# Kernel optimization log

Hardware: AMD Instinct MI355X
Metric: run time of the kernel (lower is better)

## Reference

```python
import jax, jax.numpy as jnp
import numpy as np
import math

IN_DIM = 1024
L = 4096
D_MODEL = 512
D_INNER = 1024   # expand=2 * d_model
D_STATE = 16
D_CONV = 4
DT_RANK = 32     # ceil(d_model / 16)
N_LAYERS = 2
RATE = 10


def setup_inputs() -> dict:
    key = jax.random.key(0)
    ks = iter(jax.random.split(key, 32))
    def w(shape, fan_in):
        return jax.random.normal(next(ks), shape, jnp.float32) * (1.0 / math.sqrt(fan_in))
    return {
        "x": jax.random.normal(next(ks), (1, L, IN_DIM), jnp.float32),
        "rate": RATE,
        "fc1_w": w((D_MODEL, IN_DIM), IN_DIM),
        "fc1_b": jnp.zeros((D_MODEL,), jnp.float32),
        "ln_w": jnp.ones((N_LAYERS, D_MODEL), jnp.float32),
        "ln_b": jnp.zeros((N_LAYERS, D_MODEL), jnp.float32),
        "in_proj_w": w((N_LAYERS, 2 * D_INNER, D_MODEL), D_MODEL),
        "conv_w": w((N_LAYERS, D_INNER, D_CONV), D_CONV),
        "conv_b": jnp.zeros((N_LAYERS, D_INNER), jnp.float32),
        "x_proj_w": w((N_LAYERS, DT_RANK + 2 * D_STATE, D_INNER), D_INNER),
        "dt_proj_w": w((N_LAYERS, D_INNER, DT_RANK), DT_RANK),
        "dt_proj_b": jax.random.normal(next(ks), (N_LAYERS, D_INNER), jnp.float32) * 0.1,
        "A_log": jnp.tile(jnp.log(jnp.arange(1, D_STATE + 1, dtype=jnp.float32)), (N_LAYERS, D_INNER, 1)),
        "D_skip": jnp.ones((N_LAYERS, D_INNER), jnp.float32),
        "out_proj_w": w((N_LAYERS, D_MODEL, D_INNER), D_INNER),
        "norm_w": jnp.ones((D_MODEL,), jnp.float32),
        "norm_b": jnp.zeros((D_MODEL,), jnp.float32),
        "attn_w1": w((128, D_MODEL), D_MODEL),
        "attn_b1": jnp.zeros((128,), jnp.float32),
        "attn_w2": w((1, 128), 128),
        "attn_b2": jnp.zeros((1,), jnp.float32),
        "out2048_w": w((2048, D_MODEL), D_MODEL),
        "out2048_b": jnp.zeros((2048,), jnp.float32),
    }


def _layernorm(x, w, b, eps=1e-5):
    mu = x.mean(-1, keepdims=True)
    var = ((x - mu) ** 2).mean(-1, keepdims=True)
    return (x - mu) * jax.lax.rsqrt(var + eps) * w + b


def _causal_conv(x, w, b):
    # depthwise causal conv: x [L, d], w [d, K] -> y[t, d] = sum_k w[d, k] * x[t - (K-1) + k, d]
    K = w.shape[1]
    xp = jnp.pad(x, ((K - 1, 0), (0, 0)))
    y = sum(xp[k:k + x.shape[0]] * w[:, k] for k in range(K))
    return y + b


def _selective_scan(u, dt, A, B, C, Dp, z):
    # u, dt, z: [L, d]; A: [d, n]; B, C: [L, n]; Dp: [d]
    def step(h, inp):
        dt_t, B_t, C_t, u_t = inp
        dA = jnp.exp(dt_t[:, None] * A)                    # [d, n]
        h = dA * h + (dt_t * u_t)[:, None] * B_t[None, :]  # [d, n]
        return h, h @ C_t                                  # y_t: [d]
    h0 = jnp.zeros((u.shape[1], A.shape[1]), u.dtype)
    _, y = jax.lax.scan(step, h0, (dt, B, C, u))
    return (y + u * Dp) * jax.nn.silu(z)


def _srmamba(h, perm, inv, in_w, cw, cb, xw, dtw, dtb, A_log, Dp, ow):
    xz = h @ in_w.T                         # [L, 2*d_inner]
    x, z = jnp.split(xz, 2, axis=-1)
    x, z = x[perm], z[perm]                 # sequence reordering (stride `rate`)
    x = jax.nn.silu(_causal_conv(x, cw, cb))
    dbl = x @ xw.T                          # [L, dt_rank + 2n]
    dt = jax.nn.softplus(dbl[:, :DT_RANK] @ dtw.T + dtb)
    B = dbl[:, DT_RANK:DT_RANK + D_STATE]
    C = dbl[:, DT_RANK + D_STATE:]
    y = _selective_scan(x, dt, -jnp.exp(A_log), B, C, Dp, z)
    return y[inv] @ ow.T                    # restore original order, out_proj


def reference(x, rate, fc1_w, fc1_b, ln_w, ln_b, in_proj_w, conv_w, conv_b, x_proj_w, dt_proj_w, dt_proj_b, A_log, D_skip, out_proj_w, norm_w, norm_b, attn_w1, attn_b1, attn_w2, attn_b2, out2048_w, out2048_b):
    h = jax.nn.relu(x[0] @ fc1_w.T + fc1_b)   # [L, 512]
    Lx = h.shape[0]
    perm = jnp.concatenate([jnp.arange(i, Lx, rate) for i in range(rate)])
    inv = jnp.argsort(perm)
    for l in range(N_LAYERS):
        h = h + _srmamba(_layernorm(h, ln_w[l], ln_b[l]), perm, inv,
                         in_proj_w[l], conv_w[l], conv_b[l], x_proj_w[l],
                         dt_proj_w[l], dt_proj_b[l], A_log[l], D_skip[l], out_proj_w[l])
    h = _layernorm(h, norm_w, norm_b)
    a = jnp.tanh(h @ attn_w1.T + attn_b1) @ attn_w2.T + attn_b2  # [L, 1]
    Aatt = jax.nn.softmax(a[:, 0])                                # [L]
    pooled = Aatt @ h                                             # [512]
    out = pooled @ out2048_w.T + out2048_b                        # [2048]
    return out[None, :], Aatt[None, None, :]
```

## Files before the change

kernel.cpp:

```cpp
#include <hip/hip_runtime.h>
#include <hip/hip_fp16.h>
#include <math.h>

#define L 4096
#define DIN 1024
#define DM 512
#define DI 1024
#define DS 16
#define DTR 32
#define NCH 128
#define CHK 32

typedef _Float16 v8h __attribute__((ext_vector_type(8)));
typedef float v4f __attribute__((ext_vector_type(4)));

__global__ void perm_k(int* __restrict__ perm, const int* __restrict__ ratep) {
    int p = blockIdx.x * blockDim.x + threadIdx.x;
    if (p >= L) return;
    int rate = ratep[0];
    int cum = 0;
    for (int g = 0; g < rate; ++g) {
        int sz = (L - g + rate - 1) / rate;
        if (p < cum + sz) { perm[p] = g + rate * (p - cum); return; }
        cum += sz;
    }
}

__global__ __launch_bounds__(256) void f2h_k(
    const float* __restrict__ in, _Float16* __restrict__ out)
{
    int i = (blockIdx.x * 256 + threadIdx.x) * 4;
    float4 v = *(const float4*)(in + i);
    _Float16 h4[4] = {(_Float16)v.x, (_Float16)v.y, (_Float16)v.z, (_Float16)v.w};
    *(uint2*)(out + i) = *(uint2*)h4;
}

__global__ __launch_bounds__(256) void zero4_k(float* __restrict__ p) {
    int i = (blockIdx.x * 256 + threadIdx.x) * 4;
    *(float4*)(p + i) = make_float4(0.f, 0.f, 0.f, 0.f);
}

template<int ACT, int BNT>
__global__ __launch_bounds__(256) void hgemm_nt(
    const _Float16* __restrict__ A, int lda,
    const _Float16* __restrict__ B, int ldb,
    float* __restrict__ C, int ldc,
    const float* __restrict__ bias, int K, int accum)
{
    constexpr int MI = (BNT == 128) ? 4 : 2;
    __shared__ _Float16 As[128][40];
    __shared__ _Float16 Bs[BNT][40];
    int tid = threadIdx.x;
    int m0 = blockIdx.y * 128, n0 = blockIdx.x * BNT;
    int lane = tid & 63, wave = tid >> 6;
    int wm, wn;
    if constexpr (BNT == 128) { wm = (wave >> 1) * 64; wn = (wave & 1) * 64; }
    else                      { wm = wave * 32;        wn = 0; }
    int quad = lane >> 4, r16 = lane & 15;
    v4f acc[MI][4] = {};

    int srow = tid >> 1;
    int scol = (tid & 1) * 16;
    const _Float16* Ag = A + (size_t)(m0 + srow) * lda + scol;
    int srowB = (BNT == 128) ? srow : (tid >> 2);
    int scolB = (BNT == 128) ? scol : (tid & 3) * 8;
    const _Float16* Bg = B + (size_t)(n0 + srowB) * ldb + scolB;

    uint4 a0, a1, b0, b1;
    a0 = *(const uint4*)(Ag);
    a1 = *(const uint4*)(Ag + 8);
    b0 = *(const uint4*)(Bg);
    if constexpr (BNT == 128) b1 = *(const uint4*)(Bg + 8);

    int KS = K / 32;
    for (int ks = 0; ks < KS; ++ks) {
        __syncthreads();
        *(uint4*)&As[srow][scol] = a0;
        *(uint4*)&As[srow][scol + 8] = a1;
        *(uint4*)&Bs[srowB][scolB] = b0;
        if constexpr (BNT == 128) *(uint4*)&Bs[srowB][scolB + 8] = b1;
        __syncthreads();
        if (ks + 1 < KS) {
            int k0 = (ks + 1) * 32;
            a0 = *(const uint4*)(Ag + k0);
            a1 = *(const uint4*)(Ag + k0 + 8);
            b0 = *(const uint4*)(Bg + k0);
            if constexpr (BNT == 128) b1 = *(const uint4*)(Bg + k0 + 8);
        }
        v8h af[MI], bf[4];
#pragma unroll
        for (int i = 0; i < MI; ++i)
            af[i] = *(const v8h*)&As[wm + i * 16 + r16][quad * 8];
#pragma unroll
        for (int j = 0; j < 4; ++j)
            bf[j] = *(const v8h*)&Bs[wn + j * 16 + r16][quad * 8];
#pragma unroll
        for (int i = 0; i < MI; ++i)
#pragma unroll
            for (int j = 0; j < 4; ++j)
                acc[i][j] = __builtin_amdgcn_mfma_f32_16x16x32_f16(
                    af[i], bf[j], acc[i][j], 0, 0, 0);
    }

#pragma unroll
    for (int i = 0; i < MI; ++i) {
#pragma unroll
        for (int j = 0; j < 4; ++j) {
            int col = n0 + wn + j * 16 + r16;
            int rbase = m0 + wm + i * 16 + quad * 4;
            float bv = bias ? bias[col] : 0.f;
#pragma unroll
            for (int r = 0; r < 4; ++r) {
                float v = acc[i][j][r] + bv;
                if (ACT == 1) v = fmaxf(v, 0.f);
                float* p = C + (size_t)(rbase + r) * ldc + col;
                if (accum) v += *p;
                *p = v;
            }
        }
    }
}

#define BM 64
#define BN 64
#define BKK 32
template<int ACT>
__global__ __launch_bounds__(256) void gemm_nt(
    const float* __restrict__ A, int lda,
    const float* __restrict__ B, int ldb,
    float* __restrict__ C, int ldc,
    const float* __restrict__ bias,
    int M, int N, int K, int kchunk, int accum)
{
    __shared__ float As[BKK][BM + 4];
    __shared__ float Bs[BKK][BN + 4];
    int tid = threadIdx.x;
    int m0 = blockIdx.y * BM;
    int n0 = blockIdx.x * BN;
    int tx = tid & 15, ty = tid >> 4;
    float acc[4][4] = {};
    int arow = tid >> 3;
    int ak = (tid & 7) * 4;
    int kb = blockIdx.z * kchunk;
    int ke = min(K, kb + kchunk);

    for (int k0 = kb; k0 < ke; k0 += BKK) {
#pragma unroll
        for (int r = 0; r < 2; ++r) {
            int row = arow + r * 32;
            float4 va = *(const float4*)(A + (size_t)(m0 + row) * lda + k0 + ak);
            As[ak + 0][row] = va.x; As[ak + 1][row] = va.y;
            As[ak + 2][row] = va.z; As[ak + 3][row] = va.w;
            float4 vb = *(const float4*)(B + (size_t)(n0 + row) * ldb + k0 + ak);
            Bs[ak + 0][row] = vb.x; Bs[ak + 1][row] = vb.y;
            Bs[ak + 2][row] = vb.z; Bs[ak + 3][row] = vb.w;
        }
        __syncthreads();
#pragma unroll
        for (int kk = 0; kk < BKK; ++kk) {
            float4 a4 = *(const float4*)&As[kk][ty * 4];
            float4 b4 = *(const float4*)&Bs[kk][tx * 4];
            float a[4] = {a4.x, a4.y, a4.z, a4.w};
            float b[4] = {b4.x, b4.y, b4.z, b4.w};
#pragma unroll
            for (int i = 0; i < 4; ++i)
#pragma unroll
                for (int j = 0; j < 4; ++j)
                    acc[i][j] = fmaf(a[i], b[j], acc[i][j]);
        }
        __syncthreads();
    }

#pragma unroll
    for (int i = 0; i < 4; ++i) {
        int row = m0 + ty * 4 + i;
        int col = n0 + tx * 4;
        float* cp = C + (size_t)row * ldc + col;
        if (accum == 2) {
#pragma unroll
            for (int j = 0; j < 4; ++j) atomicAdd(cp + j, acc[i][j]);
            continue;
        }
        float v[4];
#pragma unroll
        for (int j = 0; j < 4; ++j) {
            float x = acc[i][j] + (bias ? bias[col + j] : 0.f);
            if (ACT == 2) x = (x > 20.f) ? x : log1pf(expf(x));
            else if (ACT == 3) x = tanhf(x);
            v[j] = x;
        }
        if (accum == 1) {
#pragma unroll
            for (int j = 0; j < 4; ++j) v[j] += cp[j];
        }
#pragma unroll
        for (int j = 0; j < 4; ++j) cp[j] = v[j];
    }
}

__global__ __launch_bounds__(256) void layernorm_k(
    const float* __restrict__ x, const float* __restrict__ w,
    const float* __restrict__ b, float* __restrict__ o,
    _Float16* __restrict__ oh)
{
    int row = blockIdx.x;
    int tid = threadIdx.x;
    const float* xr = x + (size_t)row * DM;
    float v0 = xr[tid], v1 = xr[tid + 256];
    float s = v0 + v1, ss = v0 * v0 + v1 * v1;
    for (int off = 32; off; off >>= 1) {
        s += __shfl_down(s, off, 64);
        ss += __shfl_down(ss, off, 64);
    }
    __shared__ float sm[4], sm2[4];
    int wave = tid >> 6, lane = tid & 63;
    if (lane == 0) { sm[wave] = s; sm2[wave] = ss; }
    __syncthreads();
    float tot = sm[0] + sm[1] + sm[2] + sm[3];
    float tot2 = sm2[0] + sm2[1] + sm2[2] + sm2[3];
    float mu = tot * (1.f / DM);
    float var = tot2 * (1.f / DM) - mu * mu;
    float rs = rsqrtf(var + 1e-5f);
    float y0 = (v0 - mu) * rs * w[tid] + b[tid];
    float y1 = (v1 - mu) * rs * w[tid + 256] + b[tid + 256];
    o[(size_t)row * DM + tid] = y0;
    o[(size_t)row * DM + tid + 256] = y1;
    if (oh) {
        oh[(size_t)row * DM + tid] = (_Float16)y0;
        oh[(size_t)row * DM + tid + 256] = (_Float16)y1;
    }
}

__global__ __launch_bounds__(256) void conv_silu_k(
    const float* __restrict__ xz, const int* __restrict__ perm,
    const float* __restrict__ cw, const float* __restrict__ cb,
    float* __restrict__ xc)
{
    int g = blockIdx.x * 256 + threadIdx.x;
    int c = g & (DI - 1), p = g >> 10;
    float acc = cb[c];
#pragma unroll
    for (int k = 0; k < 4; ++k) {
        int q = p + k - 3;
        if (q >= 0)
            acc = fmaf(xz[(size_t)perm[q] * (2 * DI) + c], cw[c * 4 + k], acc);
    }
    float sig = 1.f / (1.f + __expf(-acc));
    xc[g] = acc * sig;
}

__global__ __launch_bounds__(256) void scan_pass1(
    const float* __restrict__ dt, const float* __restrict__ u,
    const float* __restrict__ dbl, const float* __restrict__ A_log,
    float* __restrict__ Aprod, float* __restrict__ carry)
{
    int c = blockIdx.x * 256 + threadIdx.x;
    int j = blockIdx.y;
    float Ac[16];
#pragma unroll
    for (int s = 0; s < 16; ++s) Ac[s] = -__expf(A_log[c * DS + s]);
    float ap[16], h[16];
#pragma unroll
    for (int s = 0; s < 16; ++s) { ap[s] = 1.f; h[s] = 0.f; }
    int t0 = j * CHK;
    for (int tt = 0; tt < CHK; ++tt) {
        int t = t0 + tt;
        float dtv = dt[(size_t)t * DI + c];
        float uv  = u[(size_t)t * DI + c];
        v4f Bv[4];
#pragma unroll
        for (int q = 0; q < 4; ++q)
            Bv[q] = *(const v4f*)(dbl + (size_t)t * 64 + DTR + q * 4);
        float du = dtv * uv;
#pragma unroll
        for (int s = 0; s < 16; ++s) {
            float dA = __expf(dtv * Ac[s]);
            h[s] = fmaf(dA, h[s], du * Bv[s >> 2][s & 3]);
            ap[s] *= dA;
        }
    }
    size_t base = ((size_t)j * DI + c) * DS;
#pragma unroll
    for (int q = 0; q < 4; ++q) {
        *(v4f*)(Aprod + base + q * 4) = *(v4f*)&ap[q * 4];
        *(v4f*)(carry + base + q * 4) = *(v4f*)&h[q * 4];
    }
}

__global__ __launch_bounds__(256) void scan_pass2(
    const float* __restrict__ Aprod, const float* __restrict__ carry,
    float* __restrict__ Hin)
{
    int idx = blockIdx.x * 256 + threadIdx.x;
    float H = 0.f;
    Hin[idx] = 0.f;
    for (int j = 1; j < NCH; ++j) {
        H = fmaf(Aprod[(size_t)(j - 1) * (DI * DS) + idx], H,
                 carry[(size_t)(j - 1) * (DI * DS) + idx]);
        Hin[(size_t)j * (DI * DS) + idx] = H;
    }
}

__global__ __launch_bounds__(256) void scan_pass3(
    const float* __restrict__ dt, const float* __restrict__ u,
    const float* __restrict__ dbl, const float* __restrict__ xz,
    const float* __restrict__ A_log, const float* __restrict__ Dsk,
    const int* __restrict__ perm, const float* __restrict__ Hin,
    _Float16* __restrict__ yo)
{
    int c = blockIdx.x * 256 + threadIdx.x;
    int j = blockIdx.y;
    float Ac[16];
#pragma unroll
    for (int s = 0; s < 16; ++s) Ac[s] = -__expf(A_log[c * DS + s]);
    float Dp = Dsk[c];
    float h[16];
    size_t hbase = ((size_t)j * DI + c) * DS;
#pragma unroll
    for (int q = 0; q < 4; ++q)
        *(v4f*)&h[q * 4] = *(const v4f*)(Hin + hbase + q * 4);
    int t0 = j * CHK;
    for (int tt = 0; tt < CHK; ++tt) {
        int t = t0 + tt;
        float dtv = dt[(size_t)t * DI + c];
        float uv  = u[(size_t)t * DI + c];
        v4f Bv[4], Cv[4];
#pragma unroll
        for (int q = 0; q < 4; ++q) {
            Bv[q] = *(const v4f*)(dbl + (size_t)t * 64 + DTR + q * 4);
            Cv[q] = *(const v4f*)(dbl + (size_t)t * 64 + DTR + DS + q * 4);
        }
        float du = dtv * uv;
        float y = 0.f;
#pragma unroll
        for (int s = 0; s < 16; ++s) {
            float dA = __expf(dtv * Ac[s]);
            h[s] = fmaf(dA, h[s], du * Bv[s >> 2][s & 3]);
            y = fmaf(h[s], Cv[s >> 2][s & 3], y);
        }
        int tp = perm[t];
        float z = xz[(size_t)tp * (2 * DI) + DI + c];
        float sig = 1.f / (1.f + __expf(-z));
        yo[(size_t)tp * DI + c] = (_Float16)((y + uv * Dp) * (z * sig));
    }
}

__global__ __launch_bounds__(256) void attnscore_k(
    const float* __restrict__ t1, const float* __restrict__ w2,
    const float* __restrict__ b2, float* __restrict__ avec)
{
    int t = blockIdx.x * 256 + threadIdx.x;
    const float* r = t1 + (size_t)t * 128;
    float acc = 0.f;
#pragma unroll 8
    for (int j = 0; j < 128; ++j) acc = fmaf(r[j], w2[j], acc);
    avec[t] = acc + b2[0];
}

__global__ __launch_bounds__(1024) void softmax_k(
    const float* __restrict__ a, float* __restrict__ out)
{
    int tid = threadIdx.x;
    float v[4];
    float mx = -1e30f;
#pragma unroll
    for (int i = 0; i < 4; ++i) { v[i] = a[tid + i * 1024]; mx = fmaxf(mx, v[i]); }
    __shared__ float sm[16];
    for (int off = 32; off; off >>= 1) mx = fmaxf(mx, __shfl_xor(mx, off, 64));
    int wave = tid >> 6, lane = tid & 63;
    if (lane == 0) sm[wave] = mx;
    __syncthreads();
    if (tid < 16) {
        float m = sm[tid];
        for (int off = 8; off; off >>= 1) m = fmaxf(m, __shfl_xor(m, off, 64));
        sm[tid] = m;
    }
    __syncthreads();
    mx = sm[0];
    float s = 0.f;
#pragma unroll
    for (int i = 0; i < 4; ++i) { v[i] = __expf(v[i] - mx); s += v[i]; }
    for (int off = 32; off; off >>= 1) s += __shfl_xor(s, off, 64);
    __syncthreads();
    if (lane == 0) sm[wave] = s;
    __syncthreads();
    if (tid < 16) {
        float t2 = sm[tid];
        for (int off = 8; off; off >>= 1) t2 += __shfl_xor(t2, off, 64);
        sm[tid] = t2;
    }
    __syncthreads();
    float inv = 1.f / sm[0];
#pragma unroll
    for (int i = 0; i < 4; ++i) out[tid + i * 1024] = v[i] * inv;
}

__global__ void zero_k(float* p, int n) {
    int i = blockIdx.x * 256 + threadIdx.x;
    if (i < n) p[i] = 0.f;
}

__global__ __launch_bounds__(512) void pool_k(
    const float* __restrict__ aatt, const float* __restrict__ h,
    float* __restrict__ pooled)
{
    int m = threadIdx.x;
    int t0 = blockIdx.x * 128;
    float acc = 0.f;
    for (int r = 0; r < 128; ++r) {
        int t = t0 + r;
        acc = fmaf(aatt[t], h[(size_t)t * DM + m], acc);
    }
    atomicAdd(&pooled[m], acc);
}

__global__ __launch_bounds__(64) void out2048_k(
    const float* __restrict__ pooled, const float* __restrict__ w,
    const float* __restrict__ b, float* __restrict__ out)
{
    int n = blockIdx.x;
    int lane = threadIdx.x;
    const float* wr = w + (size_t)n * DM;
    float acc = 0.f;
#pragma unroll
    for (int k = 0; k < 8; ++k)
        acc = fmaf(wr[lane + k * 64], pooled[lane + k * 64], acc);
    for (int off = 32; off; off >>= 1) acc += __shfl_xor(acc, off, 64);
    if (lane == 0) out[n] = acc + b[n];
}

extern "C" void kernel_launch(void* const* d_in, const int* in_sizes, int n_in,
                              void* d_out, int out_size, void* d_ws, size_t ws_size,
                              hipStream_t stream) {
    const float* x     = (const float*)d_in[0];
    const int*   rate  = (const int*)d_in[1];
    const float* fc1_w = (const float*)d_in[2];
    const float* fc1_b = (const float*)d_in[3];
    const float* ln_w  = (const float*)d_in[4];
    const float* ln_b  = (const float*)d_in[5];
    const float* ipw   = (const float*)d_in[6];
    const float* cw    = (const float*)d_in[7];
    const float* cb    = (const float*)d_in[8];
    const float* xpw   = (const float*)d_in[9];
    const float* dtw   = (const float*)d_in[10];
    const float* dtpb  = (const float*)d_in[11];
    const float* A_log = (const float*)d_in[12];
    const float* Dsk   = (const float*)d_in[13];
    const float* opw   = (const float*)d_in[14];
    const float* nw    = (const float*)d_in[15];
    const float* nb    = (const float*)d_in[16];
    const float* aw1   = (const float*)d_in[17];
    const float* ab1   = (const float*)d_in[18];
    const float* aw2   = (const float*)d_in[19];
    const float* ab2   = (const float*)d_in[20];
    const float* ow    = (const float*)d_in[21];
    const float* ob    = (const float*)d_in[22];
    float* out = (float*)d_out;

    int* perm = (int*)d_ws;
    float* f = (float*)d_ws + 4096;
    float* h    = f; f += (size_t)L * DM;
    float* hln  = f; f += (size_t)L * DM;
    float* xz   = f; f += (size_t)L * 2 * DI;
    float* xc   = f; f += (size_t)L * DI;
    float* dbl  = f; f += (size_t)L * 64;
    float* dtv  = f; f += (size_t)L * DI;
    float* t1   = f; f += (size_t)L * 128;
    float* avec = f; f += L;
    float* pooled = f; f += DM;
    float* Aprod = f; f += (size_t)NCH * DI * DS;
    float* carry = f; f += (size_t)NCH * DI * DS;
    float* Hin   = f; f += (size_t)NCH * DI * DS;
    _Float16* fh = (_Float16*)f;
    _Float16* xh     = fh; fh += (size_t)L * DIN;
    _Float16* hln_h  = fh; fh += (size_t)L * DM;
    _Float16* yo_h   = fh; fh += (size_t)L * DI;
    _Float16* fc1w_h = fh; fh += (size_t)DM * DIN;
    _Float16* ipw_h  = fh; fh += (size_t)2 * 2 * DI * DM;
    _Float16* opw_h  = fh; fh += (size_t)2 * DM * DI;

    perm_k<<<16, 256, 0, stream>>>(perm, rate);

    f2h_k<<<L * DIN / 1024, 256, 0, stream>>>(x, xh);
    f2h_k<<<DM * DIN / 1024, 256, 0, stream>>>(fc1_w, fc1w_h);
    f2h_k<<<2 * 2 * DI * DM / 1024, 256, 0, stream>>>(ipw, ipw_h);
    f2h_k<<<2 * DM * DI / 1024, 256, 0, stream>>>(opw, opw_h);

    hgemm_nt<1, 64><<<dim3(DM / 64, L / 128), 256, 0, stream>>>(
        xh, DIN, fc1w_h, DIN, h, DM, fc1_b, DIN, 0);

    for (int l = 0; l < 2; ++l) {
        layernorm_k<<<L, 256, 0, stream>>>(h, ln_w + l * DM, ln_b + l * DM, hln, hln_h);
        hgemm_nt<0, 128><<<dim3(2 * DI / 128, L / 128), 256, 0, stream>>>(
            hln_h, DM, ipw_h + (size_t)l * 2 * DI * DM, DM, xz, 2 * DI,
            nullptr, DM, 0);
        conv_silu_k<<<L * DI / 256, 256, 0, stream>>>(
            xz, perm, cw + (size_t)l * DI * 4, cb + (size_t)l * DI, xc);
        zero4_k<<<L * 64 / 1024, 256, 0, stream>>>(dbl);
        gemm_nt<0><<<dim3(1, L / 64, 4), 256, 0, stream>>>(
            xc, DI, xpw + (size_t)l * 64 * DI, DI, dbl, 64, nullptr,
            L, 64, DI, DI / 4, 2);
        gemm_nt<2><<<dim3(DI / 64, L / 64), 256, 0, stream>>>(
            dbl, 64, dtw + (size_t)l * DI * DTR, DTR, dtv, DI,
            dtpb + (size_t)l * DI, L, DI, DTR, DTR, 0);
        scan_pass1<<<dim3(DI / 256, NCH), 256, 0, stream>>>(
            dtv, xc, dbl, A_log + (size_t)l * DI * DS, Aprod, carry);
        scan_pass2<<<DI * DS / 256, 256, 0, stream>>>(Aprod, carry, Hin);
        scan_pass3<<<dim3(DI / 256, NCH), 256, 0, stream>>>(
            dtv, xc, dbl, xz, A_log + (size_t)l * DI * DS, Dsk + (size_t)l * DI,
            perm, Hin, yo_h);
        hgemm_nt<0, 64><<<dim3(DM / 64, L / 128), 256, 0, stream>>>(
            yo_h, DI, opw_h + (size_t)l * DM * DI, DI, h, DM, nullptr, DI, 1);
    }

    layernorm_k<<<L, 256, 0, stream>>>(h, nw, nb, hln, nullptr);
    gemm_nt<3><<<dim3(128 / 64, L / 64), 256, 0, stream>>>(
        hln, DM, aw1, DM, t1, 128, ab1, L, 128, DM, DM, 0);
    attnscore_k<<<L / 256, 256, 0, stream>>>(t1, aw2, ab2, avec);
    softmax_k<<<1, 1024, 0, stream>>>(avec, out + 2048);
    zero_k<<<2, 256, 0, stream>>>(pooled, DM);
    pool_k<<<32, 512, 0, stream>>>(out + 2048, hln, pooled);
    out2048_k<<<2048, 64, 0, stream>>>(pooled, ow, ob, out);
}
```

Baseline: 608.8 us.

## Load GEMM tiles directly into LDS and merge fp16 conversion launches

The half-precision GEMM now stages its A and B tiles with global_load_lds, which writes 16-byte chunks straight into shared memory instead of passing them through registers. To match the contiguous per-lane layout of that instruction, the row padding is dropped and the register-based prefetch of the next K slice is removed. The four float-to-half conversion launches are also merged into one multi-segment kernel to save launch overhead. The trade-off is that loads no longer overlap with MFMA work, and the unpadded tiles may cause LDS bank conflicts when fragments are read.

```diff
diff --git a/kernel.cpp b/kernel.cpp
--- a/kernel.cpp
+++ b/kernel.cpp
@@ -13,6 +13,12 @@
 
 typedef _Float16 v8h __attribute__((ext_vector_type(8)));
 typedef float v4f __attribute__((ext_vector_type(4)));
+
+__device__ __forceinline__ void async_cp16(const void* g, void* l) {
+    __builtin_amdgcn_global_load_lds(
+        (const __attribute__((address_space(1))) unsigned int*)g,
+        (__attribute__((address_space(3))) unsigned int*)l, 16, 0, 0);
+}
 
 __global__ void perm_k(int* __restrict__ perm, const int* __restrict__ ratep) {
     int p = blockIdx.x * blockDim.x + threadIdx.x;
@@ -26,13 +32,22 @@
     }
 }
 
-__global__ __launch_bounds__(256) void f2h_k(
-    const float* __restrict__ in, _Float16* __restrict__ out)
-{
-    int i = (blockIdx.x * 256 + threadIdx.x) * 4;
-    float4 v = *(const float4*)(in + i);
+__global__ __launch_bounds__(256) void f2h_multi_k(
+    const float* __restrict__ s0, _Float16* __restrict__ d0, int b0,
+    const float* __restrict__ s1, _Float16* __restrict__ d1, int b1,
+    const float* __restrict__ s2, _Float16* __restrict__ d2, int b2,
+    const float* __restrict__ s3, _Float16* __restrict__ d3, int b3)
+{
+    int b = blockIdx.x;
+    const float* src; _Float16* dst; int lb;
+    if (b < b0)                { src = s0; dst = d0; lb = b; }
+    else if (b < b0 + b1)      { src = s1; dst = d1; lb = b - b0; }
+    else if (b < b0 + b1 + b2) { src = s2; dst = d2; lb = b - b0 - b1; }
+    else                       { src = s3; dst = d3; lb = b - b0 - b1 - b2; }
+    int i = (lb * 256 + threadIdx.x) * 4;
+    float4 v = *(const float4*)(src + i);
     _Float16 h4[4] = {(_Float16)v.x, (_Float16)v.y, (_Float16)v.z, (_Float16)v.w};
-    *(uint2*)(out + i) = *(uint2*)h4;
+    *(uint2*)(dst + i) = *(uint2*)h4;
 }
 
 __global__ __launch_bounds__(256) void zero4_k(float* __restrict__ p) {
@@ -48,45 +63,37 @@
     const float* __restrict__ bias, int K, int accum)
 {
     constexpr int MI = (BNT == 128) ? 4 : 2;
-    __shared__ _Float16 As[128][40];
-    __shared__ _Float16 Bs[BNT][40];
+    __shared__ _Float16 As[128][32];
+    __shared__ _Float16 Bs[BNT][32];
     int tid = threadIdx.x;
+    int lane = tid & 63, wave = tid >> 6;
     int m0 = blockIdx.y * 128, n0 = blockIdx.x * BNT;
-    int lane = tid & 63, wave = tid >> 6;
     int wm, wn;
     if constexpr (BNT == 128) { wm = (wave >> 1) * 64; wn = (wave & 1) * 64; }
     else                      { wm = wave * 32;        wn = 0; }
     int quad = lane >> 4, r16 = lane & 15;
     v4f acc[MI][4] = {};
 
-    int srow = tid >> 1;
-    int scol = (tid & 1) * 16;
-    const _Float16* Ag = A + (size_t)(m0 + srow) * lda + scol;
-    int srowB = (BNT == 128) ? srow : (tid >> 2);
-    int scolB = (BNT == 128) ? scol : (tid & 3) * 8;
-    const _Float16* Bg = B + (size_t)(n0 + srowB) * ldb + scolB;
-
-    uint4 a0, a1, b0, b1;
-    a0 = *(const uint4*)(Ag);
-    a1 = *(const uint4*)(Ag + 8);
-    b0 = *(const uint4*)(Bg);
-    if constexpr (BNT == 128) b1 = *(const uint4*)(Bg + 8);
+    int lrow = lane >> 2, lcg = (lane & 3) * 8;
+    int rowA0 = wave * 16 + lrow;
+    const _Float16* pA0 = A + (size_t)(m0 + rowA0) * lda + lcg;
+    const _Float16* pA1 = A + (size_t)(m0 + 64 + rowA0) * lda + lcg;
+    const _Float16* pB0 = B + (size_t)(n0 + rowA0) * ldb + lcg;
+    const _Float16* pB1 = B + (size_t)(n0 + 64 + rowA0) * ldb + lcg;
+    _Float16* lA0 = &As[wave * 16][0];
+    _Float16* lA1 = &As[64 + wave * 16][0];
+    _Float16* lB0 = &Bs[wave * 16][0];
+    _Float16* lB1 = (BNT == 128) ? &Bs[(BNT == 128 ? 64 : 0) + wave * 16][0] : nullptr;
 
     int KS = K / 32;
     for (int ks = 0; ks < KS; ++ks) {
+        int k0 = ks * 32;
         __syncthreads();
-        *(uint4*)&As[srow][scol] = a0;
-        *(uint4*)&As[srow][scol + 8] = a1;
-        *(uint4*)&Bs[srowB][scolB] = b0;
-        if constexpr (BNT == 128) *(uint4*)&Bs[srowB][scolB + 8] = b1;
+        async_cp16(pA0 + k0, lA0);
+        async_cp16(pA1 + k0, lA1);
+        async_cp16(pB0 + k0, lB0);
+        if constexpr (BNT == 128) async_cp16(pB1 + k0, lB1);
         __syncthreads();
-        if (ks + 1 < KS) {
-            int k0 = (ks + 1) * 32;
-            a0 = *(const uint4*)(Ag + k0);
-            a1 = *(const uint4*)(Ag + k0 + 8);
-            b0 = *(const uint4*)(Bg + k0);
-            if constexpr (BNT == 128) b1 = *(const uint4*)(Bg + k0 + 8);
-        }
         v8h af[MI], bf[4];
 #pragma unroll
         for (int i = 0; i < MI; ++i)
@@ -481,10 +488,12 @@
 
     perm_k<<<16, 256, 0, stream>>>(perm, rate);
 
-    f2h_k<<<L * DIN / 1024, 256, 0, stream>>>(x, xh);
-    f2h_k<<<DM * DIN / 1024, 256, 0, stream>>>(fc1_w, fc1w_h);
-    f2h_k<<<2 * 2 * DI * DM / 1024, 256, 0, stream>>>(ipw, ipw_h);
-    f2h_k<<<2 * DM * DI / 1024, 256, 0, stream>>>(opw, opw_h);
+    f2h_multi_k<<<(L * DIN + DM * DIN + 2 * 2 * DI * DM + 2 * DM * DI) / 1024,
+                  256, 0, stream>>>(
+        x, xh, L * DIN / 1024,
+        fc1_w, fc1w_h, DM * DIN / 1024,
+        ipw, ipw_h, 2 * 2 * DI * DM / 1024,
+        opw, opw_h, 2 * DM * DI / 1024);
 
     hgemm_nt<1, 64><<<dim3(DM / 64, L / 128), 256, 0, stream>>>(
         xh, DIN, fc1w_h, DIN, h, DM, fc1_b, DIN, 0);
```

Measured after the change: 614.6 us. About the same (+1.0%).
